# Performance work log

Hardware: AMD Instinct MI355X
Metric: run time of the kernel (lower is better)

## Reference

```python
import jax, jax.numpy as jnp
import numpy as np

N = 100000
E = 1600000
D_IN = 128
D_HID = 128


def setup_inputs() -> dict:
    key = jax.random.key(0)
    ks = jax.random.split(key, 10)
    x = jax.random.normal(ks[0], (N, D_IN), dtype=jnp.float32)
    edge_index = jax.random.randint(ks[1], (2, E), 0, N, dtype=jnp.int64)
    def lin(k, i, o):
        kw, kb = jax.random.split(k)
        s = 1.0 / np.sqrt(i)
        return (jax.random.uniform(kw, (o, i), jnp.float32, -s, s),
                jax.random.uniform(kb, (o,), jnp.float32, -s, s))
    w0a, b0a = lin(ks[2], D_IN, D_HID)
    w0b, b0b = lin(ks[3], D_HID, D_HID)
    w1a, b1a = lin(ks[4], D_HID, D_HID)
    w1b, b1b = lin(ks[5], D_HID, D_HID)
    return {"x": x, "edge_index": edge_index,
            "w0a": w0a, "b0a": b0a, "w0b": w0b, "b0b": b0b,
            "w1a": w1a, "b1a": b1a, "w1b": w1b, "b1b": b1b}


def _gin_layer(x, src, dst, wa, ba, wb, bb):
    # GINConv, eps=0: h_i = x_i + sum_{j in N(i)} x_j (messages from src aggregated at dst)
    agg = jax.ops.segment_sum(x[src], dst, num_segments=N)  # [N, D]
    h = x + agg
    h = jax.nn.relu(h @ wa.T + ba)  # LinearBlock (no bn, no dropout)
    return h @ wb.T + bb            # final Linear of local_nn


def reference(x, edge_index, w0a, b0a, w0b, b0b, w1a, b1a, w1b, b1b):
    src, dst = edge_index[0], edge_index[1]
    h = _gin_layer(x, src, dst, w0a, b0a, w0b, b0b)
    h = _gin_layer(h, src, dst, w1a, b1a, w1b, b1b)
    return h
```

## Files before the change

### kernel.cpp

```cpp
#include <hip/hip_runtime.h>


typedef __attribute__((ext_vector_type(8))) short bf16x8;
typedef __attribute__((ext_vector_type(4))) float floatx4;
typedef __attribute__((ext_vector_type(2))) float floatx2;
typedef __attribute__((ext_vector_type(4))) unsigned uintx4;

#define WS_ALIGN(x) (((x) + 255) & ~(size_t)255)
#define NBMAX 400
#define BCAP 6144

__device__ __forceinline__ unsigned short f2b(float f) {
  unsigned u = __builtin_bit_cast(unsigned, f);
  u = (u + 0x7FFF + ((u >> 16) & 1)) >> 16;
  return (unsigned short)u;
}

__device__ __forceinline__ floatx2 bpair(unsigned d) {
  floatx2 r;
  r[0] = __builtin_bit_cast(float, d << 16);
  r[1] = __builtin_bit_cast(float, d & 0xffff0000u);
  return r;
}

__global__ __launch_bounds__(256) void prep_kernel(const float* __restrict__ x,
                                                   unsigned short* __restrict__ xb,
                                                   const float* __restrict__ w0a,
                                                   const float* __restrict__ w0b,
                                                   const float* __restrict__ w1a,
                                                   const float* __restrict__ w1b,
                                                   uintx4* __restrict__ wb16,
                                                   int* __restrict__ bcnt, int n4) {
  int i = blockIdx.x * 256 + threadIdx.x;
  if (i < n4) {
    float4 v = ((const float4*)x)[i];
    uint2 pk;
    pk.x = (unsigned)f2b(v.x) | ((unsigned)f2b(v.y) << 16);
    pk.y = (unsigned)f2b(v.z) | ((unsigned)f2b(v.w) << 16);
    ((uint2*)xb)[i] = pk;
  }
  if (i < 8192) {
    const float* W = (i < 2048) ? w0a : (i < 4096) ? w0b : (i < 6144) ? w1a : w1b;
    int j = i & 2047;
    float4 a = ((const float4*)W)[j * 2];
    float4 b = ((const float4*)W)[j * 2 + 1];
    uintx4 pk;
    pk.x = (unsigned)f2b(a.x) | ((unsigned)f2b(a.y) << 16);
    pk.y = (unsigned)f2b(a.z) | ((unsigned)f2b(a.w) << 16);
    pk.z = (unsigned)f2b(b.x) | ((unsigned)f2b(b.y) << 16);
    pk.w = (unsigned)f2b(b.z) | ((unsigned)f2b(b.w) << 16);
    wb16[i] = pk;
  }
  if (i < NBMAX) bcnt[i] = 0;
}

__global__ __launch_bounds__(256) void bucket_split(const int* __restrict__ src,
                                                    const int* __restrict__ dst,
                                                    int* __restrict__ bcnt,
                                                    unsigned* __restrict__ barr, int E, int nb) {
  __shared__ int cnt[NBMAX], base[NBMAX], cur[NBMAX];
  int t = threadIdx.x;
  for (int i = t; i < nb; i += 256) { cnt[i] = 0; cur[i] = 0; }
  __syncthreads();
  int e0 = blockIdx.x * 8192;
  int s[32], d[32];
  if (e0 + 8192 <= E) {
    const int4* src4 = (const int4*)src;
    const int4* dst4 = (const int4*)dst;
    int b4 = blockIdx.x * 2048;
#pragma unroll
    for (int k = 0; k < 8; k++) {
      int4 sv = src4[b4 + k * 256 + t];
      int4 dv = dst4[b4 + k * 256 + t];
      s[k * 4 + 0] = sv.x; d[k * 4 + 0] = dv.x;
      s[k * 4 + 1] = sv.y; d[k * 4 + 1] = dv.y;
      s[k * 4 + 2] = sv.z; d[k * 4 + 2] = dv.z;
      s[k * 4 + 3] = sv.w; d[k * 4 + 3] = dv.w;
    }
  } else {
#pragma unroll
    for (int k = 0; k < 32; k++) {
      int e = e0 + k * 256 + t;
      if (e < E) { s[k] = src[e]; d[k] = dst[e]; } else { d[k] = -1; }
    }
  }
#pragma unroll
  for (int k = 0; k < 32; k++)
    if (d[k] >= 0) atomicAdd(&cnt[d[k] >> 8], 1);
  __syncthreads();
  for (int i = t; i < nb; i += 256) base[i] = cnt[i] ? atomicAdd(&bcnt[i], cnt[i]) : 0;
  __syncthreads();
#pragma unroll
  for (int k = 0; k < 32; k++)
    if (d[k] >= 0) {
      int b = d[k] >> 8;
      int r = atomicAdd(&cur[b], 1);
      barr[(size_t)b * BCAP + base[b] + r] = ((unsigned)(d[k] & 255) << 17) | (unsigned)s[k];
    }
}

__global__ __launch_bounds__(256) void bucket_csr(const unsigned* __restrict__ barr,
                                                  const int* __restrict__ bcnt,
                                                  int* __restrict__ rowptr, int* __restrict__ srt,
                                                  int n, int nb) {
  __shared__ int cnt[256], off[256], off2[256], red[256];
  int b = blockIdx.x, t = threadIdx.x;
  int cb = bcnt[b];
  int node0 = b * 256;
  int nlocal = min(256, n - node0);
  cnt[t] = 0;
  off2[t] = 0;
  int partial = 0;
  for (int i = t; i < b; i += 256) partial += bcnt[i];
  red[t] = partial;
  __syncthreads();
  for (int o = 128; o > 0; o >>= 1) {
    if (t < o) red[t] += red[t + o];
    __syncthreads();
  }
  int sb = red[0];

  const unsigned* bp = barr + (size_t)b * BCAP;
  const uint4* bp4 = (const uint4*)bp;
  int cb4 = cb >> 2;
  for (int i = t; i < cb4; i += 256) {
    uint4 v4 = bp4[i];
    atomicAdd(&cnt[v4.x >> 17], 1);
    atomicAdd(&cnt[v4.y >> 17], 1);
    atomicAdd(&cnt[v4.z >> 17], 1);
    atomicAdd(&cnt[v4.w >> 17], 1);
  }
  for (int i = cb4 * 4 + t; i < cb; i += 256) atomicAdd(&cnt[bp[i] >> 17], 1);
  __syncthreads();
  int v = cnt[t];
  off[t] = v;
  __syncthreads();
  for (int o = 1; o < 256; o <<= 1) {
    int add = (t >= o) ? off[t - o] : 0;
    __syncthreads();
    off[t] += add;
    __syncthreads();
  }
  int excl = off[t] - v;
  if (t < nlocal) rowptr[node0 + t] = sb + excl;
  cnt[t] = excl;
  __syncthreads();
  for (int i = t; i < cb4; i += 256) {
    uint4 v4 = bp4[i];
    unsigned pks[4] = {v4.x, v4.y, v4.z, v4.w};
#pragma unroll
    for (int j = 0; j < 4; j++) {
      int local = pks[j] >> 17;
      int r = atomicAdd(&off2[local], 1);
      srt[sb + cnt[local] + r] = pks[j] & 0x1FFFF;
    }
  }
  for (int i = cb4 * 4 + t; i < cb; i += 256) {
    unsigned pk = bp[i];
    int local = pk >> 17;
    int r = atomicAdd(&off2[local], 1);
    srt[sb + cnt[local] + r] = pk & 0x1FFFF;
  }
  if (b == nb - 1 && t == 0) rowptr[n] = sb + cb;
}

__global__ __launch_bounds__(256) void aggregate_bf16(const unsigned short* __restrict__ X,
                                                      const int* __restrict__ rowptr,
                                                      const int* __restrict__ srt,
                                                      unsigned short* __restrict__ out, int n) {
  int w = blockIdx.x * 4 + (threadIdx.x >> 6);
  if (w >= n) return;
  int lane = threadIdx.x & 63;
  int c = lane & 15;
  int s = lane >> 4;
  const uintx4* Xv = (const uintx4*)X;

  int p0 = rowptr[w], e = rowptr[w + 1];
  int deg = e - p0;
  int trips = (deg + 3) >> 2;

  uintx4 uself = {0, 0, 0, 0};
  if (s == 0) uself = Xv[(size_t)w * 16 + c];

  floatx2 acc2[4];
#pragma unroll
  for (int i = 0; i < 4; i++) acc2[i] = floatx2{0.f, 0.f};

  for (int g = 0; g < trips; g += 4) {
    int idx[4];
    bool val[4];
#pragma unroll
    for (int k = 0; k < 4; k++) {
      int j = (g + k) * 4 + s;
      val[k] = j < deg;
      idx[k] = srt[p0 + (val[k] ? j : 0)];
    }
    uintx4 u[4];
#pragma unroll
    for (int k = 0; k < 4; k++) u[k] = Xv[(size_t)idx[k] * 16 + c];
#pragma unroll
    for (int k = 0; k < 4; k++) {
      if (!val[k]) u[k] = uintx4{0, 0, 0, 0};
      acc2[0] += bpair(u[k].x);
      acc2[1] += bpair(u[k].y);
      acc2[2] += bpair(u[k].z);
      acc2[3] += bpair(u[k].w);
    }
  }

  acc2[0] += bpair(uself.x);
  acc2[1] += bpair(uself.y);
  acc2[2] += bpair(uself.z);
  acc2[3] += bpair(uself.w);

#pragma unroll
  for (int i = 0; i < 4; i++) {
#pragma unroll
    for (int k = 0; k < 2; k++) {
      acc2[i][k] += __shfl_xor(acc2[i][k], 16, 64);
      acc2[i][k] += __shfl_xor(acc2[i][k], 32, 64);
    }
  }

  unsigned pk = (unsigned)f2b(acc2[s][0]) | ((unsigned)f2b(acc2[s][1]) << 16);
  ((unsigned*)out)[(size_t)w * 64 + c * 4 + s] = pk;
}

__device__ __forceinline__ void stage_wb(char* buf, const uintx4* __restrict__ Wb, int t) {
  for (int idx = t; idx < 2048; idx += 512) {
    int nrow = idx >> 4, c = idx & 15;
    uintx4 pk = Wb[idx];
    *(uintx4*)(buf + nrow * 256 + ((c ^ (nrow & 15)) << 4)) = pk;
  }
}

template <int OUT_BF16>
__global__ __launch_bounds__(512) void mlp_kernel(
    const unsigned short* __restrict__ A, const uintx4* __restrict__ Wa16,
    const float* __restrict__ ba, const uintx4* __restrict__ Wb16,
    const float* __restrict__ bb, void* __restrict__ Cout, int n) {
  __shared__ __align__(16) char lds[65536];
  char* bufA = lds;
  char* bufB = lds + 32768;
  int t = threadIdx.x;
  stage_wb(bufA, Wa16, t);
  stage_wb(bufB, Wb16, t);

  int wave = t >> 6, lane = t & 63;
  int m = lane & 15, q = lane >> 4;
  int rbase = blockIdx.x * 128;
  int rowA = rbase + wave * 16 + m;
  int rA = rowA < n ? rowA : (n - 1);

  bf16x8 af[4];
  const bf16x8* Arow = (const bf16x8*)(A + (size_t)rA * 128);
#pragma unroll
  for (int ks = 0; ks < 4; ks++) af[ks] = Arow[ks * 4 + q];

  __syncthreads();

  floatx4 acc[8];
  floatx4 zf = {0.f, 0.f, 0.f, 0.f};
#pragma unroll
  for (int j = 0; j < 8; j++) acc[j] = zf;
#pragma unroll
  for (int ks = 0; ks < 4; ks++) {
#pragma unroll
    for (int j = 0; j < 8; j++) {
      bf16x8 bf = *(const bf16x8*)(bufA + (j * 16 + m) * 256 + (((ks * 4 + q) ^ m) << 4));
      acc[j] = __builtin_amdgcn_mfma_f32_16x16x32_bf16(af[ks], bf, acc[j], 0, 0, 0);
    }
  }
  __syncthreads();

#pragma unroll
  for (int j = 0; j < 8; j++) {
    float bias = ba[j * 16 + m];
#pragma unroll
    for (int reg = 0; reg < 4; reg++) {
      float v = fmaxf(acc[j][reg] + bias, 0.f);
      int lr = wave * 16 + q * 4 + reg;
      int col = j * 16 + m;
      *(unsigned short*)(bufA + lr * 256 + (((col >> 3) ^ (lr & 15)) << 4) + (col & 7) * 2) =
          f2b(v);
    }
  }
  __syncthreads();

  int lrA = wave * 16 + m;
#pragma unroll
  for (int ks = 0; ks < 4; ks++)
    af[ks] = *(const bf16x8*)(bufA + lrA * 256 + (((ks * 4 + q) ^ m) << 4));
#pragma unroll
  for (int j = 0; j < 8; j++) acc[j] = zf;
#pragma unroll
  for (int ks = 0; ks < 4; ks++) {
#pragma unroll
    for (int j = 0; j < 8; j++) {
      bf16x8 bf = *(const bf16x8*)(bufB + (j * 16 + m) * 256 + (((ks * 4 + q) ^ m) << 4));
      acc[j] = __builtin_amdgcn_mfma_f32_16x16x32_bf16(af[ks], bf, acc[j], 0, 0, 0);
    }
  }

  __syncthreads();
  int nrows = min(128, n - rbase);
  if (OUT_BF16) {
#pragma unroll
    for (int j = 0; j < 8; j++) {
      float bias = bb[j * 16 + m];
#pragma unroll
      for (int reg = 0; reg < 4; reg++) {
        int lr = wave * 16 + q * 4 + reg;
        int col = j * 16 + m;
        *(unsigned short*)(bufA + lr * 256 + col * 2) = f2b(acc[j][reg] + bias);
      }
    }
    __syncthreads();
    const uintx4* sv = (const uintx4*)bufA;
    uintx4* gout = (uintx4*)((unsigned short*)Cout + (size_t)rbase * 128);
    int chunks = nrows * 16;
    for (int i = t; i < chunks; i += 512) gout[i] = sv[i];
  } else {
    float* stg = (float*)lds;
#pragma unroll
    for (int j = 0; j < 8; j++) {
      float bias = bb[j * 16 + m];
#pragma unroll
      for (int reg = 0; reg < 4; reg++) {
        int lr = wave * 16 + q * 4 + reg;
        int col = j * 16 + m;
        stg[lr * 128 + col] = acc[j][reg] + bias;
      }
    }
    __syncthreads();
    const uintx4* sv = (const uintx4*)lds;
    uintx4* gout = (uintx4*)((float*)Cout + (size_t)rbase * 128);
    int chunks = nrows * 32;
    for (int i = t; i < chunks; i += 512) gout[i] = sv[i];
  }
}

extern "C" void kernel_launch(void* const* d_in, const int* in_sizes, int n_in,
                              void* d_out, int out_size, void* d_ws, size_t ws_size,
                              hipStream_t stream) {
  const float* x   = (const float*)d_in[0];
  const int*   ei  = (const int*)d_in[1];
  const float* w0a = (const float*)d_in[2];
  const float* b0a = (const float*)d_in[3];
  const float* w0b = (const float*)d_in[4];
  const float* b0b = (const float*)d_in[5];
  const float* w1a = (const float*)d_in[6];
  const float* b1a = (const float*)d_in[7];
  const float* w1b = (const float*)d_in[8];
  const float* b1b = (const float*)d_in[9];
  float* out = (float*)d_out;

  int n = in_sizes[0] / 128;
  int E = in_sizes[1] / 2;
  const int* src = ei;
  const int* dst = ei + E;
  int nb = (n + 255) / 256;

  char* w = (char*)d_ws;
  int* rowptr = (int*)w;           w += WS_ALIGN((size_t)(n + 1) * 4);
  int* bcnt = (int*)w;             w += WS_ALIGN((size_t)NBMAX * 4);
  int* srt = (int*)w;              w += WS_ALIGN((size_t)E * 4);
  unsigned short* xb = (unsigned short*)w;  w += WS_ALIGN((size_t)n * 128 * 2);
  uintx4* wb16 = (uintx4*)w;       w += WS_ALIGN((size_t)8192 * 16);
  unsigned* barr = (unsigned*)w;
  unsigned short* B1 = (unsigned short*)w;

  int n4 = n * 32;

  prep_kernel<<<(n4 + 255) / 256, 256, 0, stream>>>(x, xb, w0a, w0b, w1a, w1b, wb16, bcnt, n4);

  bucket_split<<<(E + 8191) / 8192, 256, 0, stream>>>(src, dst, bcnt, barr, E, nb);
  bucket_csr<<<nb, 256, 0, stream>>>(barr, bcnt, rowptr, srt, n, nb);

  int agg_grid = (n + 3) / 4;
  int mlp_grid = (n + 127) / 128;

  aggregate_bf16<<<agg_grid, 256, 0, stream>>>(xb, rowptr, srt, (unsigned short*)B1, n);
  mlp_kernel<1><<<mlp_grid, 512, 0, stream>>>(B1, wb16, b0a, wb16 + 2048, b0b, xb, n);

  aggregate_bf16<<<agg_grid, 256, 0, stream>>>(xb, rowptr, srt, (unsigned short*)B1, n);
  mlp_kernel<0><<<mlp_grid, 512, 0, stream>>>(B1, wb16 + 4096, b1a, wb16 + 6144, b1b, out, n);
}
```

Before: 305.4 us.

## Fuse bucket split into prep kernel and deepen aggregate gather unroll

Merges the bf16 conversion/weight packing kernel and the edge bucket-split kernel into one launch, with the first blocks doing the bucketing and the rest doing the conversion. The bucket counter reset moves to a hipMemsetAsync. The aggregation kernel now issues six neighbor gathers per iteration instead of four and gets a launch-bounds occupancy hint. The aim is to drop a kernel boundary and raise memory-level parallelism in the gather, at the cost of an extra memset call and higher register pressure.

```diff
diff --git a/kernel.cpp b/kernel.cpp
--- a/kernel.cpp
+++ b/kernel.cpp
@@ -23,15 +23,56 @@
   return r;
 }
 
-__global__ __launch_bounds__(256) void prep_kernel(const float* __restrict__ x,
-                                                   unsigned short* __restrict__ xb,
-                                                   const float* __restrict__ w0a,
-                                                   const float* __restrict__ w0b,
-                                                   const float* __restrict__ w1a,
-                                                   const float* __restrict__ w1b,
-                                                   uintx4* __restrict__ wb16,
-                                                   int* __restrict__ bcnt, int n4) {
-  int i = blockIdx.x * 256 + threadIdx.x;
+__global__ __launch_bounds__(256) void prep_split_kernel(
+    const float* __restrict__ x, unsigned short* __restrict__ xb,
+    const float* __restrict__ w0a, const float* __restrict__ w0b,
+    const float* __restrict__ w1a, const float* __restrict__ w1b,
+    uintx4* __restrict__ wb16, const int* __restrict__ src,
+    const int* __restrict__ dst, int* __restrict__ bcnt,
+    unsigned* __restrict__ barr, int E, int n4, int nsb) {
+  __shared__ int cnt[NBMAX], base[NBMAX], cur[NBMAX];
+  int t = threadIdx.x;
+  if (blockIdx.x < nsb) {
+    for (int i = t; i < NBMAX; i += 256) { cnt[i] = 0; cur[i] = 0; }
+    __syncthreads();
+    int e0 = blockIdx.x * 8192;
+    int s[32], d[32];
+    if (e0 + 8192 <= E) {
+      const int4* src4 = (const int4*)src;
+      const int4* dst4 = (const int4*)dst;
+      int b4 = blockIdx.x * 2048;
+#pragma unroll
+      for (int k = 0; k < 8; k++) {
+        int4 sv = src4[b4 + k * 256 + t];
+        int4 dv = dst4[b4 + k * 256 + t];
+        s[k * 4 + 0] = sv.x; d[k * 4 + 0] = dv.x;
+        s[k * 4 + 1] = sv.y; d[k * 4 + 1] = dv.y;
+        s[k * 4 + 2] = sv.z; d[k * 4 + 2] = dv.z;
+        s[k * 4 + 3] = sv.w; d[k * 4 + 3] = dv.w;
+      }
+    } else {
+#pragma unroll
+      for (int k = 0; k < 32; k++) {
+        int e = e0 + k * 256 + t;
+        if (e < E) { s[k] = src[e]; d[k] = dst[e]; } else { d[k] = -1; }
+      }
+    }
+#pragma unroll
+    for (int k = 0; k < 32; k++)
+      if (d[k] >= 0) atomicAdd(&cnt[d[k] >> 8], 1);
+    __syncthreads();
+    for (int i = t; i < NBMAX; i += 256) base[i] = cnt[i] ? atomicAdd(&bcnt[i], cnt[i]) : 0;
+    __syncthreads();
+#pragma unroll
+    for (int k = 0; k < 32; k++)
+      if (d[k] >= 0) {
+        int b = d[k] >> 8;
+        int r = atomicAdd(&cur[b], 1);
+        barr[(size_t)b * BCAP + base[b] + r] = ((unsigned)(d[k] & 255) << 17) | (unsigned)s[k];
+      }
+    return;
+  }
+  int i = (blockIdx.x - nsb) * 256 + t;
   if (i < n4) {
     float4 v = ((const float4*)x)[i];
     uint2 pk;
@@ -51,52 +92,6 @@
     pk.w = (unsigned)f2b(b.z) | ((unsigned)f2b(b.w) << 16);
     wb16[i] = pk;
   }
-  if (i < NBMAX) bcnt[i] = 0;
-}
-
-__global__ __launch_bounds__(256) void bucket_split(const int* __restrict__ src,
-                                                    const int* __restrict__ dst,
-                                                    int* __restrict__ bcnt,
-                                                    unsigned* __restrict__ barr, int E, int nb) {
-  __shared__ int cnt[NBMAX], base[NBMAX], cur[NBMAX];
-  int t = threadIdx.x;
-  for (int i = t; i < nb; i += 256) { cnt[i] = 0; cur[i] = 0; }
-  __syncthreads();
-  int e0 = blockIdx.x * 8192;
-  int s[32], d[32];
-  if (e0 + 8192 <= E) {
-    const int4* src4 = (const int4*)src;
-    const int4* dst4 = (const int4*)dst;
-    int b4 = blockIdx.x * 2048;
-#pragma unroll
-    for (int k = 0; k < 8; k++) {
-      int4 sv = src4[b4 + k * 256 + t];
-      int4 dv = dst4[b4 + k * 256 + t];
-      s[k * 4 + 0] = sv.x; d[k * 4 + 0] = dv.x;
-      s[k * 4 + 1] = sv.y; d[k * 4 + 1] = dv.y;
-      s[k * 4 + 2] = sv.z; d[k * 4 + 2] = dv.z;
-      s[k * 4 + 3] = sv.w; d[k * 4 + 3] = dv.w;
-    }
-  } else {
-#pragma unroll
-    for (int k = 0; k < 32; k++) {
-      int e = e0 + k * 256 + t;
-      if (e < E) { s[k] = src[e]; d[k] = dst[e]; } else { d[k] = -1; }
-    }
-  }
-#pragma unroll
-  for (int k = 0; k < 32; k++)
-    if (d[k] >= 0) atomicAdd(&cnt[d[k] >> 8], 1);
-  __syncthreads();
-  for (int i = t; i < nb; i += 256) base[i] = cnt[i] ? atomicAdd(&bcnt[i], cnt[i]) : 0;
-  __syncthreads();
-#pragma unroll
-  for (int k = 0; k < 32; k++)
-    if (d[k] >= 0) {
-      int b = d[k] >> 8;
-      int r = atomicAdd(&cur[b], 1);
-      barr[(size_t)b * BCAP + base[b] + r] = ((unsigned)(d[k] & 255) << 17) | (unsigned)s[k];
-    }
 }
 
 __global__ __launch_bounds__(256) void bucket_csr(const unsigned* __restrict__ barr,
@@ -164,10 +159,11 @@
   if (b == nb - 1 && t == 0) rowptr[n] = sb + cb;
 }
 
-__global__ __launch_bounds__(256) void aggregate_bf16(const unsigned short* __restrict__ X,
-                                                      const int* __restrict__ rowptr,
-                                                      const int* __restrict__ srt,
-                                                      unsigned short* __restrict__ out, int n) {
+__global__ __launch_bounds__(256, 8) void aggregate_bf16(const unsigned short* __restrict__ X,
+                                                         const int* __restrict__ rowptr,
+                                                         const int* __restrict__ srt,
+                                                         unsigned short* __restrict__ out,
+                                                         int n) {
   int w = blockIdx.x * 4 + (threadIdx.x >> 6);
   if (w >= n) return;
   int lane = threadIdx.x & 63;
@@ -186,20 +182,20 @@
 #pragma unroll
   for (int i = 0; i < 4; i++) acc2[i] = floatx2{0.f, 0.f};
 
-  for (int g = 0; g < trips; g += 4) {
-    int idx[4];
-    bool val[4];
-#pragma unroll
-    for (int k = 0; k < 4; k++) {
+  for (int g = 0; g < trips; g += 6) {
+    int idx[6];
+    bool val[6];
+#pragma unroll
+    for (int k = 0; k < 6; k++) {
       int j = (g + k) * 4 + s;
       val[k] = j < deg;
       idx[k] = srt[p0 + (val[k] ? j : 0)];
     }
-    uintx4 u[4];
-#pragma unroll
-    for (int k = 0; k < 4; k++) u[k] = Xv[(size_t)idx[k] * 16 + c];
-#pragma unroll
-    for (int k = 0; k < 4; k++) {
+    uintx4 u[6];
+#pragma unroll
+    for (int k = 0; k < 6; k++) u[k] = Xv[(size_t)idx[k] * 16 + c];
+#pragma unroll
+    for (int k = 0; k < 6; k++) {
       if (!val[k]) u[k] = uintx4{0, 0, 0, 0};
       acc2[0] += bpair(u[k].x);
       acc2[1] += bpair(u[k].y);
@@ -371,10 +367,12 @@
   unsigned short* B1 = (unsigned short*)w;
 
   int n4 = n * 32;
-
-  prep_kernel<<<(n4 + 255) / 256, 256, 0, stream>>>(x, xb, w0a, w0b, w1a, w1b, wb16, bcnt, n4);
-
-  bucket_split<<<(E + 8191) / 8192, 256, 0, stream>>>(src, dst, bcnt, barr, E, nb);
+  int nsb = (E + 8191) / 8192;
+  int ncvt = (n4 + 255) / 256;
+
+  hipMemsetAsync(bcnt, 0, (size_t)NBMAX * 4, stream);
+  prep_split_kernel<<<nsb + ncvt, 256, 0, stream>>>(
+      x, xb, w0a, w0b, w1a, w1b, wb16, src, dst, bcnt, barr, E, n4, nsb);
   bucket_csr<<<nb, 256, 0, stream>>>(barr, bcnt, rowptr, srt, n, nb);
 
   int agg_grid = (n + 3) / 4;
```

After: 313.8 us. 2.7% more time.
